# Kernel optimization log

Hardware: AMD Instinct MI355X
Metric: run time of the kernel (lower is better)

Reference implementation:

```python
import jax, jax.numpy as jnp
import numpy as np

B, C, N = 64, 512, 3000
GH, GW = 90, 50          # coordinate grid the points are sampled from
MAX_H, MAX_W = 70, 40    # module max_height / max_width
N_VALID = 2800           # points per sample with ys > -1


def setup_inputs() -> dict:
    key = jax.random.key(0)
    kf, kp = jax.random.split(key)
    features = jax.random.normal(kf, (B, C, N), dtype=jnp.float32)
    # unique grid cells per batch item -> no duplicate scatter targets
    perms = jax.vmap(lambda k: jax.random.permutation(k, GH * GW)[:N])(
        jax.random.split(kp, B))  # (B, N)
    ys = (perms // GW).astype(jnp.int32)
    xs = (perms % GW).astype(jnp.int32)
    valid = jnp.arange(N) < N_VALID
    ys = jnp.where(valid[None, :], ys, -1)  # invalid points marked ys == -1
    return {"features": features, "ys": ys, "xs": xs}


def reference(features, ys, xs):
    # Eval-mode (validation=True) forward: deterministic centered crop/pad.
    mask = ys > -1  # (B, N) real points
    BIG = 1_000_000
    min_y = jnp.where(mask, ys, BIG).min(axis=1)
    min_x = jnp.where(mask, xs, BIG).min(axis=1)
    max_y = jnp.where(mask, ys, -BIG).max(axis=1)
    max_x = jnp.where(mask, xs, -BIG).max(axis=1)
    h = max_y - min_y + 1
    w = max_x - min_x + 1
    swap = w > h  # transpose tmp map when wider than tall
    H0 = jnp.where(swap, w, h)
    W0 = jnp.where(swap, h, w)
    # per-point coords inside the (possibly transposed) tmp map
    r = jnp.where(swap[:, None], xs - min_x[:, None], ys - min_y[:, None])
    c = jnp.where(swap[:, None], ys - min_y[:, None], xs - min_x[:, None])
    h_dif = H0 - MAX_H
    w_dif = W0 - MAX_W
    cut_top = jnp.where(h_dif > 0, (h_dif + 1) // 2, 0)   # ceil(h_dif/2)
    pad_top = jnp.where(h_dif > 0, 0, (-h_dif + 1) // 2)  # ceil(-h_dif/2)
    cut_left = jnp.where(w_dif > 0, (w_dif + 1) // 2, 0)
    # NOTE: original passes (pad_right, pad_left, ...) to F.pad, so the
    # computed 'pad_right' = ceil(-w_dif/2) is applied as LEFT padding.
    left_pad = jnp.where(w_dif > 0, 0, (-w_dif + 1) // 2)
    rr = r - cut_top[:, None] + pad_top[:, None]
    cc = c - cut_left[:, None] + left_pad[:, None]
    in_bounds = mask & (rr >= 0) & (rr < MAX_H) & (cc >= 0) & (cc < MAX_W)
    rr = jnp.where(in_bounds, rr, MAX_H)  # push cropped/invalid points OOB
    cc = jnp.where(in_bounds, cc, MAX_W)
    canvas = jnp.full((B, C, MAX_H, MAX_W), -1.0, dtype=features.dtype)
    bi = jnp.arange(B)[:, None]  # (B, 1)
    # scatter: canvas[b, :, rr[b,n], cc[b,n]] = features[b, :, n]
    canvas = canvas.at[bi, :, rr, cc].set(jnp.swapaxes(features, 1, 2),
                                          mode="drop")
    real2d = jnp.all(canvas != -1.0, axis=1)  # (B, H, W)
    # f_map is zeros (use_dummy_feature=False): blend = mask * canvas
    return jnp.where(real2d[:, None, :, :], canvas, jnp.zeros((), features.dtype))
```

## Files before the change

### kernel.cpp

```cpp
#include <hip/hip_runtime.h>
#include <stdint.h>

#define NB 64
#define NC 512
#define NPTS 3000
#define MAXH 70
#define MAXW 40
#define HW (MAXH * MAXW)
#define CPB 32
#define THREADS 256
#define FIXCAP 8192
#define NV4 (NPTS / 4)
#define OV4 (HW / 4)

__device__ __forceinline__ void gload_lds16(const void* g, void* l) {
    __builtin_amdgcn_global_load_lds(
        (const __attribute__((address_space(1))) uint32_t*)g,
        (__attribute__((address_space(3))) uint32_t*)l,
        16, 0, 0);
}

__global__ void fm_zero_cnt(int* cnt) {
    if (threadIdx.x == 0) cnt[0] = 0;
}

__launch_bounds__(THREADS)
__global__ void fm_gather_kernel(const float* __restrict__ feat,
                                 const int* __restrict__ ys,
                                 const int* __restrict__ xs,
                                 float* __restrict__ out,
                                 int* __restrict__ fix_cnt,
                                 int* __restrict__ fix_list,
                                 int fix_cap)
{
    __shared__ int    inv_s[HW];
    __shared__ float4 fbuf[2][NV4];
    __shared__ int    s_red[16];
    __shared__ int    s_par[5];

    const int blocks_per_b = NC / CPB;
    const int b   = blockIdx.x / blocks_per_b;
    const int c0  = (blockIdx.x % blocks_per_b) * CPB;
    const int tid = threadIdx.x;
    const int lane = tid & 63;
    const int wid  = tid >> 6;

    const int* ysb = ys + b * NPTS;
    const int* xsb = xs + b * NPTS;
    int* ybuf = (int*)fbuf[0];
    int* xbuf = (int*)fbuf[1];

    int vminY = 0x7fffffff, vminX = 0x7fffffff;
    int vmaxY = -0x7fffffff, vmaxX = -0x7fffffff;
    for (int i = tid; i < NV4; i += THREADS) {
        int4 ya = ((const int4*)ysb)[i];
        int4 xa = ((const int4*)xsb)[i];
        ((int4*)ybuf)[i] = ya;
        ((int4*)xbuf)[i] = xa;
        int yv[4] = {ya.x, ya.y, ya.z, ya.w};
        int xv[4] = {xa.x, xa.y, xa.z, xa.w};
#pragma unroll
        for (int j = 0; j < 4; ++j) {
            if (yv[j] > -1) {
                vminY = min(vminY, yv[j]); vmaxY = max(vmaxY, yv[j]);
                vminX = min(vminX, xv[j]); vmaxX = max(vmaxX, xv[j]);
            }
        }
    }
    for (int i = tid; i < HW; i += THREADS) inv_s[i] = -1;
#pragma unroll
    for (int off = 32; off > 0; off >>= 1) {
        vminY = min(vminY, __shfl_xor(vminY, off));
        vmaxY = max(vmaxY, __shfl_xor(vmaxY, off));
        vminX = min(vminX, __shfl_xor(vminX, off));
        vmaxX = max(vmaxX, __shfl_xor(vmaxX, off));
    }
    if (lane == 0) {
        s_red[wid]      = vminY;
        s_red[4  + wid] = vmaxY;
        s_red[8  + wid] = vminX;
        s_red[12 + wid] = vmaxX;
    }
    __syncthreads();
    if (tid == 0) {
        int mnY = min(min(s_red[0], s_red[1]),   min(s_red[2],  s_red[3]));
        int mxY = max(max(s_red[4], s_red[5]),   max(s_red[6],  s_red[7]));
        int mnX = min(min(s_red[8], s_red[9]),   min(s_red[10], s_red[11]));
        int mxX = max(max(s_red[12], s_red[13]), max(s_red[14], s_red[15]));
        int h = mxY - mnY + 1;
        int w = mxX - mnX + 1;
        int swap = (w > h) ? 1 : 0;
        int H0 = swap ? w : h;
        int W0 = swap ? h : w;
        int h_dif = H0 - MAXH;
        int w_dif = W0 - MAXW;
        int cut_top  = (h_dif > 0) ? (h_dif + 1) / 2 : 0;
        int pad_top  = (h_dif > 0) ? 0 : (-h_dif + 1) / 2;
        int cut_left = (w_dif > 0) ? (w_dif + 1) / 2 : 0;
        int left_pad = (w_dif > 0) ? 0 : (-w_dif + 1) / 2;
        s_par[0] = swap;
        s_par[1] = mnY;
        s_par[2] = mnX;
        s_par[3] = pad_top - cut_top;
        s_par[4] = left_pad - cut_left;
    }
    __syncthreads();

    {
        const int swp = s_par[0], mnY = s_par[1], mnX = s_par[2];
        const int roff = s_par[3], coff = s_par[4];
        for (int n = tid; n < NPTS; n += THREADS) {
            int y = ybuf[n];
            int x = xbuf[n];
            if (y > -1) {
                int r  = swp ? (x - mnX) : (y - mnY);
                int cl = swp ? (y - mnY) : (x - mnX);
                int rr = r + roff;
                int cc = cl + coff;
                if (rr >= 0 && rr < MAXH && cc >= 0 && cc < MAXW)
                    inv_s[rr * MAXW + cc] = n;
            }
        }
    }
    __syncthreads();

    int nreg[3][4];
#pragma unroll
    for (int it = 0; it < 3; ++it) {
        int i4 = it * THREADS + tid;
        if (i4 < OV4) {
#pragma unroll
            for (int j = 0; j < 4; ++j) nreg[it][j] = inv_s[i4 * 4 + j];
        }
    }
    {
        const float4* src = (const float4*)(feat + (size_t)(b * NC + c0) * NPTS);
#pragma unroll
        for (int it = 0; it < 3; ++it) {
            int i = it * THREADS + tid;
            if (i < NV4) gload_lds16(src + i, &fbuf[0][i]);
        }
    }
    __syncthreads();

    for (int ci = 0; ci < CPB; ++ci) {
        const int cur = ci & 1;
        if (ci + 1 < CPB) {
            const float4* src =
                (const float4*)(feat + (size_t)(b * NC + c0 + ci + 1) * NPTS);
#pragma unroll
            for (int it = 0; it < 3; ++it) {
                int i = it * THREADS + tid;
                if (i < NV4) gload_lds16(src + i, &fbuf[cur ^ 1][i]);
            }
        }
        const float* fp = (const float*)fbuf[cur];
        float* orow = out + (size_t)(b * NC + c0 + ci) * HW;
#pragma unroll
        for (int it = 0; it < 3; ++it) {
            int i4 = it * THREADS + tid;
            if (i4 < OV4) {
                float4 v;
                float* vp = &v.x;
#pragma unroll
                for (int j = 0; j < 4; ++j) {
                    int n = nreg[it][j];
                    float val = 0.0f;
                    if (n >= 0) {
                        val = fp[n];
                        if (val == -1.0f) {
                            int pos = atomicAdd(fix_cnt, 1);
                            if (pos < fix_cap) fix_list[pos] = b * HW + i4 * 4 + j;
                        }
                    }
                    vp[j] = val;
                }
                ((float4*)orow)[i4] = v;
            }
        }
        __syncthreads();
    }
}

__global__ void fm_fixup_kernel(const int* __restrict__ fix_cnt,
                                const int* __restrict__ fix_list,
                                int fix_cap,
                                float* __restrict__ out)
{
    int count = min(fix_cnt[0], fix_cap);
    long total = (long)count * NC;
    long stride = (long)gridDim.x * blockDim.x;
    for (long t = (long)blockIdx.x * blockDim.x + threadIdx.x; t < total; t += stride) {
        int e = (int)(t / NC);
        int c = (int)(t % NC);
        int cell = fix_list[e];
        int b   = cell / HW;
        int pos = cell % HW;
        out[(size_t)(b * NC + c) * HW + pos] = 0.0f;
    }
}

extern "C" void kernel_launch(void* const* d_in, const int* in_sizes, int n_in,
                              void* d_out, int out_size, void* d_ws, size_t ws_size,
                              hipStream_t stream) {
    const float* feat = (const float*)d_in[0];
    const int*   ys   = (const int*)d_in[1];
    const int*   xs   = (const int*)d_in[2];
    float* out = (float*)d_out;

    int* fix_cnt  = (int*)d_ws;
    int* fix_list = (int*)((char*)d_ws + 16);
    int fix_cap = 0;
    if (ws_size > 16) {
        size_t avail = (ws_size - 16) / 4;
        fix_cap = (int)((avail < FIXCAP) ? avail : FIXCAP);
    }

    fm_zero_cnt<<<1, 64, 0, stream>>>(fix_cnt);

    int grid = NB * (NC / CPB);
    fm_gather_kernel<<<grid, THREADS, 0, stream>>>(feat, ys, xs, out,
                                                   fix_cnt, fix_list, fix_cap);

    fm_fixup_kernel<<<128, 256, 0, stream>>>(fix_cnt, fix_list, fix_cap, out);
}
```

Measured before the change: 177.3 us.

## Give each wave its own double-buffered channel pipeline without block barriers

Each of the four waves in a block now streams its own 32 channels through a private double buffer in LDS. Per-wave s_waitcnt replaces the block-wide __syncthreads, removing barrier stalls between channels. The block now covers 128 channels, so the grid shrinks to 256 blocks and LDS use per block grows to about 110 KB. That limits occupancy to roughly one block, or four waves, per CU, which may hurt memory-latency hiding in this bandwidth-bound copy.

```diff
diff --git a/kernel.cpp b/kernel.cpp
--- a/kernel.cpp
+++ b/kernel.cpp
@@ -7,11 +7,14 @@
 #define MAXH 70
 #define MAXW 40
 #define HW (MAXH * MAXW)
-#define CPB 32
 #define THREADS 256
+#define WAVES 4
+#define CPB 128
+#define CPW (CPB / WAVES)
+#define NV4 750
+#define NV4P 768
+#define OV4 (HW / 4)
 #define FIXCAP 8192
-#define NV4 (NPTS / 4)
-#define OV4 (HW / 4)
 
 __device__ __forceinline__ void gload_lds16(const void* g, void* l) {
     __builtin_amdgcn_global_load_lds(
@@ -34,7 +37,7 @@
                                  int fix_cap)
 {
     __shared__ int    inv_s[HW];
-    __shared__ float4 fbuf[2][NV4];
+    __shared__ float4 fbuf[WAVES * 2 * NV4P];
     __shared__ int    s_red[16];
     __shared__ int    s_par[5];
 
@@ -43,12 +46,12 @@
     const int c0  = (blockIdx.x % blocks_per_b) * CPB;
     const int tid = threadIdx.x;
     const int lane = tid & 63;
-    const int wid  = tid >> 6;
+    const int w    = tid >> 6;
 
     const int* ysb = ys + b * NPTS;
     const int* xsb = xs + b * NPTS;
-    int* ybuf = (int*)fbuf[0];
-    int* xbuf = (int*)fbuf[1];
+    int* ybuf = (int*)fbuf;
+    int* xbuf = (int*)(fbuf + NV4P);
 
     int vminY = 0x7fffffff, vminX = 0x7fffffff;
     int vmaxY = -0x7fffffff, vmaxX = -0x7fffffff;
@@ -76,10 +79,10 @@
         vmaxX = max(vmaxX, __shfl_xor(vmaxX, off));
     }
     if (lane == 0) {
-        s_red[wid]      = vminY;
-        s_red[4  + wid] = vmaxY;
-        s_red[8  + wid] = vminX;
-        s_red[12 + wid] = vmaxX;
+        s_red[w]      = vminY;
+        s_red[4  + w] = vmaxY;
+        s_red[8  + w] = vminX;
+        s_red[12 + w] = vmaxX;
     }
     __syncthreads();
     if (tid == 0) {
@@ -88,10 +91,10 @@
         int mnX = min(min(s_red[8], s_red[9]),   min(s_red[10], s_red[11]));
         int mxX = max(max(s_red[12], s_red[13]), max(s_red[14], s_red[15]));
         int h = mxY - mnY + 1;
-        int w = mxX - mnX + 1;
-        int swap = (w > h) ? 1 : 0;
-        int H0 = swap ? w : h;
-        int W0 = swap ? h : w;
+        int w_ = mxX - mnX + 1;
+        int swap = (w_ > h) ? 1 : 0;
+        int H0 = swap ? w_ : h;
+        int W0 = swap ? h : w_;
         int h_dif = H0 - MAXH;
         int w_dif = W0 - MAXW;
         int cut_top  = (h_dif > 0) ? (h_dif + 1) / 2 : 0;
@@ -124,41 +127,51 @@
     }
     __syncthreads();
 
-    int nreg[3][4];
-#pragma unroll
-    for (int it = 0; it < 3; ++it) {
-        int i4 = it * THREADS + tid;
+    int nreg[11][4];
+#pragma unroll
+    for (int it = 0; it < 11; ++it) {
+        int i4 = it * 64 + lane;
         if (i4 < OV4) {
 #pragma unroll
             for (int j = 0; j < 4; ++j) nreg[it][j] = inv_s[i4 * 4 + j];
         }
     }
+
+    float4* buf0 = fbuf + (size_t)w * 2 * NV4P;
+    float4* buf1 = buf0 + NV4P;
+    const int cw0 = c0 + w * CPW;
+
     {
-        const float4* src = (const float4*)(feat + (size_t)(b * NC + c0) * NPTS);
-#pragma unroll
-        for (int it = 0; it < 3; ++it) {
-            int i = it * THREADS + tid;
-            if (i < NV4) gload_lds16(src + i, &fbuf[0][i]);
-        }
-    }
-    __syncthreads();
-
-    for (int ci = 0; ci < CPB; ++ci) {
-        const int cur = ci & 1;
-        if (ci + 1 < CPB) {
+        const float4* src = (const float4*)(feat + (size_t)(b * NC + cw0) * NPTS);
+#pragma unroll
+        for (int it = 0; it < 12; ++it) {
+            int i = it * 64 + lane;
+            int s = (i < NV4) ? i : (NV4 - 1);
+            gload_lds16(src + s, buf0 + i);
+        }
+    }
+
+    for (int ci = 0; ci < CPW; ++ci) {
+        asm volatile("s_waitcnt vmcnt(0)" ::: "memory");
+        __builtin_amdgcn_sched_barrier(0);
+
+        if (ci + 1 < CPW) {
             const float4* src =
-                (const float4*)(feat + (size_t)(b * NC + c0 + ci + 1) * NPTS);
-#pragma unroll
-            for (int it = 0; it < 3; ++it) {
-                int i = it * THREADS + tid;
-                if (i < NV4) gload_lds16(src + i, &fbuf[cur ^ 1][i]);
-            }
-        }
-        const float* fp = (const float*)fbuf[cur];
-        float* orow = out + (size_t)(b * NC + c0 + ci) * HW;
-#pragma unroll
-        for (int it = 0; it < 3; ++it) {
-            int i4 = it * THREADS + tid;
+                (const float4*)(feat + (size_t)(b * NC + cw0 + ci + 1) * NPTS);
+            float4* bnext = ((ci + 1) & 1) ? buf1 : buf0;
+#pragma unroll
+            for (int it = 0; it < 12; ++it) {
+                int i = it * 64 + lane;
+                int s = (i < NV4) ? i : (NV4 - 1);
+                gload_lds16(src + s, bnext + i);
+            }
+        }
+
+        const float* fp = (const float*)((ci & 1) ? buf1 : buf0);
+        float4* orow = (float4*)(out + (size_t)(b * NC + cw0 + ci) * HW);
+#pragma unroll
+        for (int it = 0; it < 11; ++it) {
+            int i4 = it * 64 + lane;
             if (i4 < OV4) {
                 float4 v;
                 float* vp = &v.x;
@@ -175,10 +188,9 @@
                     }
                     vp[j] = val;
                 }
-                ((float4*)orow)[i4] = v;
-            }
-        }
-        __syncthreads();
+                orow[i4] = v;
+            }
+        }
     }
 }
 
```

After: 240.2 us. 1.35x slower.

## Triple-buffer LDS feature rows with counted vmcnt waits and a single barrier

Applied to the files above, without the earlier changes.

Swaps the double buffer plus separate inverse-index array for a three-slot LDS ring that reuses the index slot as a feature buffer. Each channel iteration now uses one explicit vmcnt wait and one raw s_barrier instead of a trailing __syncthreads, so the next row's global-to-LDS load stays in flight while the current row is processed. Loads are padded to a fixed count per thread so the vmcnt accounting is uniform. The waits rely on hand-counted outstanding memory operations, including the output stores, which is fragile if the compiler reorders or changes the instruction count.

```diff
diff --git a/kernel.cpp b/kernel.cpp
--- a/kernel.cpp
+++ b/kernel.cpp
@@ -7,11 +7,12 @@
 #define MAXH 70
 #define MAXW 40
 #define HW (MAXH * MAXW)
+#define THREADS 256
 #define CPB 32
-#define THREADS 256
+#define NV4 750
+#define NV4P 768
+#define OV4 (HW / 4)
 #define FIXCAP 8192
-#define NV4 (NPTS / 4)
-#define OV4 (HW / 4)
 
 __device__ __forceinline__ void gload_lds16(const void* g, void* l) {
     __builtin_amdgcn_global_load_lds(
@@ -33,8 +34,7 @@
                                  int* __restrict__ fix_list,
                                  int fix_cap)
 {
-    __shared__ int    inv_s[HW];
-    __shared__ float4 fbuf[2][NV4];
+    __shared__ float4 tb[3][NV4P];
     __shared__ int    s_red[16];
     __shared__ int    s_par[5];
 
@@ -43,12 +43,13 @@
     const int c0  = (blockIdx.x % blocks_per_b) * CPB;
     const int tid = threadIdx.x;
     const int lane = tid & 63;
-    const int wid  = tid >> 6;
+    const int w    = tid >> 6;
 
     const int* ysb = ys + b * NPTS;
     const int* xsb = xs + b * NPTS;
-    int* ybuf = (int*)fbuf[0];
-    int* xbuf = (int*)fbuf[1];
+    int* ybuf = (int*)tb[0];
+    int* xbuf = (int*)tb[1];
+    int* inv  = (int*)tb[2];
 
     int vminY = 0x7fffffff, vminX = 0x7fffffff;
     int vmaxY = -0x7fffffff, vmaxX = -0x7fffffff;
@@ -67,7 +68,7 @@
             }
         }
     }
-    for (int i = tid; i < HW; i += THREADS) inv_s[i] = -1;
+    for (int i = tid; i < HW; i += THREADS) inv[i] = -1;
 #pragma unroll
     for (int off = 32; off > 0; off >>= 1) {
         vminY = min(vminY, __shfl_xor(vminY, off));
@@ -76,10 +77,10 @@
         vmaxX = max(vmaxX, __shfl_xor(vmaxX, off));
     }
     if (lane == 0) {
-        s_red[wid]      = vminY;
-        s_red[4  + wid] = vmaxY;
-        s_red[8  + wid] = vminX;
-        s_red[12 + wid] = vmaxX;
+        s_red[w]      = vminY;
+        s_red[4  + w] = vmaxY;
+        s_red[8  + w] = vminX;
+        s_red[12 + w] = vmaxX;
     }
     __syncthreads();
     if (tid == 0) {
@@ -87,11 +88,11 @@
         int mxY = max(max(s_red[4], s_red[5]),   max(s_red[6],  s_red[7]));
         int mnX = min(min(s_red[8], s_red[9]),   min(s_red[10], s_red[11]));
         int mxX = max(max(s_red[12], s_red[13]), max(s_red[14], s_red[15]));
-        int h = mxY - mnY + 1;
-        int w = mxX - mnX + 1;
-        int swap = (w > h) ? 1 : 0;
-        int H0 = swap ? w : h;
-        int W0 = swap ? h : w;
+        int h  = mxY - mnY + 1;
+        int w_ = mxX - mnX + 1;
+        int swap = (w_ > h) ? 1 : 0;
+        int H0 = swap ? w_ : h;
+        int W0 = swap ? h : w_;
         int h_dif = H0 - MAXH;
         int w_dif = W0 - MAXW;
         int cut_top  = (h_dif > 0) ? (h_dif + 1) / 2 : 0;
@@ -118,7 +119,7 @@
                 int rr = r + roff;
                 int cc = cl + coff;
                 if (rr >= 0 && rr < MAXH && cc >= 0 && cc < MAXW)
-                    inv_s[rr * MAXW + cc] = n;
+                    inv[rr * MAXW + cc] = n;
             }
         }
     }
@@ -130,32 +131,48 @@
         int i4 = it * THREADS + tid;
         if (i4 < OV4) {
 #pragma unroll
-            for (int j = 0; j < 4; ++j) nreg[it][j] = inv_s[i4 * 4 + j];
-        }
-    }
+            for (int j = 0; j < 4; ++j) nreg[it][j] = inv[i4 * 4 + j];
+        }
+    }
+    __syncthreads();
+
     {
         const float4* src = (const float4*)(feat + (size_t)(b * NC + c0) * NPTS);
 #pragma unroll
         for (int it = 0; it < 3; ++it) {
             int i = it * THREADS + tid;
-            if (i < NV4) gload_lds16(src + i, &fbuf[0][i]);
-        }
-    }
-    __syncthreads();
-
+            int s = (i < NV4) ? i : (NV4 - 1);
+            gload_lds16(src + s, tb[0] + i);
+        }
+    }
+
+    int cur = 0;
     for (int ci = 0; ci < CPB; ++ci) {
-        const int cur = ci & 1;
+        const int nxt = (cur == 2) ? 0 : cur + 1;
         if (ci + 1 < CPB) {
             const float4* src =
                 (const float4*)(feat + (size_t)(b * NC + c0 + ci + 1) * NPTS);
+            float4* bn = tb[nxt];
 #pragma unroll
             for (int it = 0; it < 3; ++it) {
                 int i = it * THREADS + tid;
-                if (i < NV4) gload_lds16(src + i, &fbuf[cur ^ 1][i]);
-            }
-        }
-        const float* fp = (const float*)fbuf[cur];
-        float* orow = out + (size_t)(b * NC + c0 + ci) * HW;
+                int s = (i < NV4) ? i : (NV4 - 1);
+                gload_lds16(src + s, bn + i);
+            }
+        }
+        if (ci == 0) {
+            asm volatile("s_waitcnt vmcnt(3)" ::: "memory");
+        } else if (ci + 1 < CPB) {
+            asm volatile("s_waitcnt vmcnt(5)" ::: "memory");
+        } else {
+            asm volatile("s_waitcnt vmcnt(2)" ::: "memory");
+        }
+        __builtin_amdgcn_sched_barrier(0);
+        __builtin_amdgcn_s_barrier();
+        __builtin_amdgcn_sched_barrier(0);
+
+        const float* fp = (const float*)tb[cur];
+        float4* orow = (float4*)(out + (size_t)(b * NC + c0 + ci) * HW);
 #pragma unroll
         for (int it = 0; it < 3; ++it) {
             int i4 = it * THREADS + tid;
@@ -175,10 +192,10 @@
                     }
                     vp[j] = val;
                 }
-                ((float4*)orow)[i4] = v;
-            }
-        }
-        __syncthreads();
+                orow[i4] = v;
+            }
+        }
+        cur = nxt;
     }
 }
 
```

Result: faster. 171.4 us (-3.3%).
